# Kernel tuning notes

Hardware: AMD Instinct MI355X
Metric: run time of the kernel (lower is better)

Reference implementation:

```python
import jax, jax.numpy as jnp
import numpy as np

B, S, D, H = 2, 2048, 1024, 16
DH = D // H  # 64


def _rotate_half(t):
    x1, x2 = jnp.split(t, 2, axis=-1)
    return jnp.concatenate([-x2, x1], axis=-1)


def setup_inputs() -> dict:
    key = jax.random.key(0)
    ks = jax.random.split(key, 11)
    x = jax.random.normal(ks[0], (B, S, D), dtype=jnp.float32)
    mask = jax.random.randint(ks[1], (B, S), 0, 2, dtype=jnp.int32)
    scale = 0.02
    wq = jax.random.normal(ks[2], (D, D), dtype=jnp.float32) * scale
    bq = jnp.zeros((D,), dtype=jnp.float32)
    wk = jax.random.normal(ks[3], (D, D), dtype=jnp.float32) * scale
    bk = jnp.zeros((D,), dtype=jnp.float32)
    wv = jax.random.normal(ks[4], (D, D), dtype=jnp.float32) * scale
    bv = jnp.zeros((D,), dtype=jnp.float32)
    wo = jax.random.normal(ks[5], (D, D), dtype=jnp.float32) * scale
    bo = jnp.zeros((D,), dtype=jnp.float32)
    return {"x": x, "mask": mask, "wq": wq, "bq": bq, "wk": wk, "bk": bk,
            "wv": wv, "bv": bv, "wo": wo, "bo": bo}


def reference(x, mask, wq, bq, wk, bk, wv, bv, wo, bo):
    b, s, d = x.shape
    # QKV projections, split heads -> [B, H, S, DH]
    q = (x @ wq + bq).reshape(b, s, H, DH).transpose(0, 2, 1, 3)
    k = (x @ wk + bk).reshape(b, s, H, DH).transpose(0, 2, 1, 3)
    v = (x @ wv + bv).reshape(b, s, H, DH).transpose(0, 2, 1, 3)
    # RoPE exactly as in source: repeat(cos,2) paired with half-split rotate
    pos = jnp.arange(s, dtype=jnp.float32)
    inv_freq = 1.0 / (10000.0 ** (jnp.arange(0, DH, 2, dtype=jnp.float32) / DH))
    angle = pos[:, None] * inv_freq[None, :]            # [S, DH/2]
    cos = jnp.repeat(jnp.cos(angle), 2, axis=-1)[None, None]  # [1,1,S,DH]
    sin = jnp.repeat(jnp.sin(angle), 2, axis=-1)[None, None]
    q = q * cos + _rotate_half(q) * sin
    k = k * cos + _rotate_half(k) * sin
    # scaled dot-product attention with additive mask
    logits = jnp.einsum('bhqd,bhkd->bhqk', q, k) / jnp.sqrt(jnp.float32(DH))
    m = mask.astype(jnp.float32)[:, None, None, :]      # [B,1,1,S]
    logits = logits + m * (-1e9)
    attn = jax.nn.softmax(logits, axis=-1)
    out = jnp.einsum('bhqk,bhkd->bhqd', attn, v)
    out = out.transpose(0, 2, 1, 3).reshape(b, s, d)
    return out @ wo + bo
```

## Files before the change

### kernel.cpp

```cpp
#include <hip/hip_runtime.h>
#include <math.h>

#define BB 2
#define SS 2048
#define DD 1024
#define HH 16

typedef unsigned short u16;
using bf16x8 = __attribute__((ext_vector_type(8))) short;
using f32x4  = __attribute__((ext_vector_type(4))) float;

#define LOG2E 1.44269504f


__device__ __forceinline__ u16 f2bf(float f) {
    unsigned u = __float_as_uint(f);
    unsigned r = u + 0x7fffu + ((u >> 16) & 1u);
    return (u16)(r >> 16);
}

__device__ __forceinline__ void gload_lds16(const void* g, const void* l) {
    __builtin_amdgcn_global_load_lds(
        (const __attribute__((address_space(1))) unsigned int*)(unsigned long long)g,
        (__attribute__((address_space(3))) unsigned int*)(unsigned int)(unsigned long long)l,
        16, 0, 0);
}

__global__ void rope_table(float* __restrict__ cost, float* __restrict__ sint) {
    int idx = blockIdx.x * 256 + threadIdx.x;
    int j   = idx >> 11;
    int pos = idx & 2047;
    double inv = pow(10000.0, -(double)j / 32.0);
    double ang = (double)pos * inv;
    cost[idx] = (float)cos(ang);
    sint[idx] = (float)sin(ang);
}

__global__ void mkbias(const int* __restrict__ mask, float* __restrict__ mb) {
    int i = blockIdx.x * 256 + threadIdx.x;
    mb[i] = -1.44269504e9f * (float)mask[i];
}

__global__ void cvt_x(const float* __restrict__ x, u16* __restrict__ xb) {
    int i = (blockIdx.x * 256 + threadIdx.x) * 4;
    float4 v = *(const float4*)(x + i);
    ushort4 o;
    o.x = f2bf(v.x); o.y = f2bf(v.y); o.z = f2bf(v.z); o.w = f2bf(v.w);
    *(ushort4*)(xb + i) = o;
}

__global__ void transpose_w(const float* __restrict__ w0, const float* __restrict__ w1,
                            const float* __restrict__ w2, const float* __restrict__ w3,
                            u16* __restrict__ o0, u16* __restrict__ o1,
                            u16* __restrict__ o2, u16* __restrict__ o3) {
    const float* in = (blockIdx.z == 0) ? w0 : (blockIdx.z == 1) ? w1 : (blockIdx.z == 2) ? w2 : w3;
    u16* out        = (blockIdx.z == 0) ? o0 : (blockIdx.z == 1) ? o1 : (blockIdx.z == 2) ? o2 : o3;
    __shared__ float t[32][33];
    int n = blockIdx.x * 32 + threadIdx.x;
    for (int i = threadIdx.y; i < 32; i += 8)
        t[i][threadIdx.x] = in[(size_t)(blockIdx.y * 32 + i) * 1024 + n];
    __syncthreads();
    int k = blockIdx.y * 32 + threadIdx.x;
    for (int i = threadIdx.y; i < 32; i += 8)
        out[(size_t)(blockIdx.x * 32 + i) * 1024 + k] = f2bf(t[threadIdx.x][i]);
}

__global__ __launch_bounds__(256)
void qkv_gemm(const u16* __restrict__ xb,
              const u16* __restrict__ wtq, const u16* __restrict__ wtk, const u16* __restrict__ wtv,
              const float* __restrict__ bq, const float* __restrict__ bk, const float* __restrict__ bv,
              const float* __restrict__ cost, const float* __restrict__ sint,
              u16* __restrict__ qo, u16* __restrict__ ko, u16* __restrict__ vo)
{
    __shared__ u16 Al[128 * 32];
    __shared__ u16 Bl[128 * 32];

    int bx = blockIdx.x;
    int which = bx >> 3;
    int n0 = (bx & 7) << 7;
    int m0 = blockIdx.y << 7;
    const u16*  wt    = (which == 0) ? wtq : (which == 1) ? wtk : wtv;
    const float* bias = (which == 0) ? bq  : (which == 1) ? bk  : bv;

    int t = threadIdx.x;
    int wid = t >> 6, lane = t & 63;
    int wr = wid >> 1, wc = wid & 1;
    int fr = lane & 15, fq = lane >> 4;

    f32x4 acc[4][4];
    #pragma unroll
    for (int m = 0; m < 4; ++m)
        #pragma unroll
        for (int n = 0; n < 4; ++n)
            #pragma unroll
            for (int r = 0; r < 4; ++r) acc[m][n][r] = 0.f;

    int srow = (lane >> 2);
    int skof = (lane & 3) << 3;

    for (int k0 = 0; k0 < 1024; k0 += 32) {
        __syncthreads();
        #pragma unroll
        for (int c = 0; c < 2; ++c) {
            int chunk = wid * 2 + c;
            int row = (chunk << 4) + srow;
            gload_lds16(xb + (size_t)(m0 + row) * 1024 + k0 + skof, &Al[chunk << 9]);
            gload_lds16(wt + (size_t)(n0 + row) * 1024 + k0 + skof, &Bl[chunk << 9]);
        }
        __syncthreads();

        bf16x8 af[4], bf[4];
        #pragma unroll
        for (int m = 0; m < 4; ++m)
            af[m] = *(const bf16x8*)&Al[((wr << 6) + (m << 4) + fr) * 32 + (fq << 3)];
        #pragma unroll
        for (int n = 0; n < 4; ++n)
            bf[n] = *(const bf16x8*)&Bl[((wc << 6) + (n << 4) + fr) * 32 + (fq << 3)];
        #pragma unroll
        for (int m = 0; m < 4; ++m)
            #pragma unroll
            for (int n = 0; n < 4; ++n)
                acc[m][n] = __builtin_amdgcn_mfma_f32_16x16x32_bf16(af[m], bf[n], acc[m][n], 0, 0, 0);
    }

    if (which < 2) {
        u16* outp = (which == 0) ? qo : ko;
        const float qs = (which == 0) ? 0.125f * LOG2E : 1.0f;
        #pragma unroll
        for (int n = 0; n < 2; ++n) {
            int col = n0 + (wc << 6) + (n << 4) + fr;
            int h = col >> 6;
            int d = col & 63;
            float b1 = bias[col], b2 = bias[col + 32];
            int a1 = d >> 1;
            #pragma unroll
            for (int mm = 0; mm < 4; ++mm) {
                int mi0 = m0 + (wr << 6) + (mm << 4) + (fq << 2);
                int bi = mi0 >> 11, s0 = mi0 & 2047;
                float4 c1 = *(const float4*)(cost + (a1 << 11) + s0);
                float4 s1 = *(const float4*)(sint + (a1 << 11) + s0);
                float4 c2 = *(const float4*)(cost + ((a1 + 16) << 11) + s0);
                float4 s2 = *(const float4*)(sint + ((a1 + 16) << 11) + s0);
                const float* c1p = (const float*)&c1;
                const float* s1p = (const float*)&s1;
                const float* c2p = (const float*)&c2;
                const float* s2p = (const float*)&s2;
                #pragma unroll
                for (int j = 0; j < 4; ++j) {
                    float x1 = acc[mm][n][j]     + b1;
                    float x2 = acc[mm][n + 2][j] + b2;
                    size_t base = ((size_t)(bi * HH + h) * SS + s0 + j) << 6;
                    outp[base + d]      = f2bf((x1 * c1p[j] - x2 * s1p[j]) * qs);
                    outp[base + d + 32] = f2bf((x2 * c2p[j] + x1 * s2p[j]) * qs);
                }
            }
        }
    } else {
        #pragma unroll
        for (int n = 0; n < 4; ++n) {
            int col = n0 + (wc << 6) + (n << 4) + fr;
            int h = col >> 6, d = col & 63;
            float bb = bias[col];
            #pragma unroll
            for (int mm = 0; mm < 4; ++mm) {
                #pragma unroll
                for (int j = 0; j < 4; ++j) {
                    int mi = m0 + (wr << 6) + (mm << 4) + (fq << 2) + j;
                    int bi = mi >> 11, s = mi & 2047;
                    vo[(((size_t)(bi * HH + h) * SS + s) << 6) + d] = f2bf(acc[mm][n][j] + bb);
                }
            }
        }
    }
}

__global__ __launch_bounds__(256)
void transpose_v(const u16* __restrict__ vin, u16* __restrict__ vout) {
    __shared__ u16 Ld[64][72];
    int stile = blockIdx.x;
    int bh    = blockIdx.y;
    int t = threadIdx.x;
    int r = t >> 2, seg = (t & 3) << 4;
    const u16* src = vin + (((size_t)bh * SS + (stile << 6) + r) << 6) + seg;
    *(uint4*)&Ld[r][seg]     = *(const uint4*)src;
    *(uint4*)&Ld[r][seg + 8] = *(const uint4*)(src + 8);
    __syncthreads();
    u16 tmp[16];
    #pragma unroll
    for (int i = 0; i < 16; ++i) tmp[i] = Ld[seg + i][r];
    u16* dst = vout + ((size_t)(bh << 6) + r) * SS + (stile << 6) + seg;
    *(uint4*)dst       = *(const uint4*)&tmp[0];
    *(uint4*)(dst + 8) = *(const uint4*)&tmp[8];
}

__global__ __launch_bounds__(256, 4)
void attn(const u16* __restrict__ qb, const u16* __restrict__ kb, const u16* __restrict__ vt,
          const float* __restrict__ mbias, u16* __restrict__ preb)
{
    __shared__ u16 Kl[2][4096];
    __shared__ u16 Vl[2][4096];
    __shared__ u16 Pl[4][1024];

    const int bid = blockIdx.x;
    const int xcd = bid & 7;
    const int idx = bid >> 3;
    const int bh  = (xcd << 2) | (idx >> 5);
    const int qb0 = (idx & 31) << 6;
    const int b   = bh >> 4;
    const int t   = threadIdx.x;
    const int w   = t >> 6;
    const int lane = t & 63;
    const int fr  = lane & 15;
    const int fq  = lane >> 4;
    const int swz = (fr & 7) << 4;

    const char* kbase = (const char*)(kb + ((size_t)bh << 17));
    const char* vbase = (const char*)(vt + ((size_t)bh << 17));
    const float* mbp  = mbias + (b << 11);

    const int sbo = ((t & 7) << 4) ^ (((t >> 3) & 7) << 4);

    const int qrow = qb0 + (w << 4) + fr;
    const u16* qp = qb + (((size_t)bh << 11) + qrow) * 64 + (fq << 3);
    bf16x8 qf0 = *(const bf16x8*)qp;
    bf16x8 qf1 = *(const bf16x8*)(qp + 32);

    f32x4 o[4];
    #pragma unroll
    for (int n = 0; n < 4; ++n)
        #pragma unroll
        for (int r = 0; r < 4; ++r) o[n][r] = 0.f;
    float mrun = -INFINITY, lrun = 0.f;

    auto STAGE = [&](int buf, int kt) {
        #pragma unroll
        for (int c = 0; c < 2; ++c) {
            int row = (c << 5) + (t >> 3);
            gload_lds16(kbase + ((size_t)(kt << 6) + row) * 128 + sbo,
                        (const char*)&Kl[buf][0] + (c << 12) + t * 16);
            gload_lds16(vbase + (size_t)row * 4096 + (kt << 7) + sbo,
                        (const char*)&Vl[buf][0] + (c << 12) + t * 16);
        }
    };

    STAGE(0, 0);
    __syncthreads();

    for (int kt = 0; kt < 32; ++kt) {
        const int cur = kt & 1;

        if (kt < 31) STAGE(cur ^ 1, kt + 1);

        f32x4 sv[4];
        #pragma unroll
        for (int g = 0; g < 4; ++g)
            #pragma unroll
            for (int r = 0; r < 4; ++r) sv[g][r] = 0.f;

        const char* Kb = (const char*)&Kl[cur][0];
        __builtin_amdgcn_s_setprio(1);
        #pragma unroll
        for (int g = 0; g < 4; ++g) {
            int row = (g << 4) + fr;
            bf16x8 kf0 = *(const bf16x8*)(Kb + row * 128 + ((fq << 4) ^ swz));
            bf16x8 kf1 = *(const bf16x8*)(Kb + row * 128 + (((fq << 4) + 64) ^ swz));
            sv[g] = __builtin_amdgcn_mfma_f32_16x16x32_bf16(kf0, qf0, sv[g], 0, 0, 0);
            sv[g] = __builtin_amdgcn_mfma_f32_16x16x32_bf16(kf1, qf1, sv[g], 0, 0, 0);
        }
        __builtin_amdgcn_s_setprio(0);

        float tm = -INFINITY;
        #pragma unroll
        for (int g = 0; g < 4; ++g) {
            const float4 m4 = *(const float4*)(mbp + (kt << 6) + (g << 4) + (fq << 2));
            sv[g][0] += m4.x; sv[g][1] += m4.y; sv[g][2] += m4.z; sv[g][3] += m4.w;
            tm = fmaxf(tm, fmaxf(fmaxf(sv[g][0], sv[g][1]), fmaxf(sv[g][2], sv[g][3])));
        }
        tm = fmaxf(tm, __shfl_xor(tm, 16));
        tm = fmaxf(tm, __shfl_xor(tm, 32));

        if (!__all(tm <= mrun + 11.0f)) {
            float newm = fmaxf(mrun, tm);
            float scale = __builtin_amdgcn_exp2f(mrun - newm);
            lrun *= scale;
            #pragma unroll
            for (int j = 0; j < 4; ++j) {
                float sj = __shfl(scale, (lane & 48) + (fq << 2) + j);
                #pragma unroll
                for (int n = 0; n < 4; ++n) o[n][j] *= sj;
            }
            mrun = newm;
        }

        float ps = 0.f;
        #pragma unroll
        for (int g = 0; g < 4; ++g) {
            float p0 = __builtin_amdgcn_exp2f(sv[g][0] - mrun);
            float p1 = __builtin_amdgcn_exp2f(sv[g][1] - mrun);
            float p2 = __builtin_amdgcn_exp2f(sv[g][2] - mrun);
            float p3 = __builtin_amdgcn_exp2f(sv[g][3] - mrun);
            ps += (p0 + p1) + (p2 + p3);
            unsigned r0, r1;
            asm("v_cvt_pk_bf16_f32 %0, %1, %2" : "=v"(r0) : "v"(p0), "v"(p1));
            asm("v_cvt_pk_bf16_f32 %0, %1, %2" : "=v"(r1) : "v"(p2), "v"(p3));
            uint2 pw; pw.x = r0; pw.y = r1;
            *(uint2*)((char*)&Pl[w][0] + fr * 128 + (((g << 5) + (fq << 3)) ^ swz)) = pw;
        }
        ps += __shfl_xor(ps, 16);
        ps += __shfl_xor(ps, 32);
        lrun += ps;

        __builtin_amdgcn_s_setprio(1);
        #pragma unroll
        for (int kk = 0; kk < 2; ++kk) {
            bf16x8 pa = *(const bf16x8*)((const char*)&Pl[w][0] + fr * 128 + (((fq << 4) + (kk << 6)) ^ swz));
            #pragma unroll
            for (int n = 0; n < 4; ++n) {
                int row = (n << 4) + fr;
                bf16x8 vf = *(const bf16x8*)((const char*)&Vl[cur][0] + row * 128 + (((fq << 4) + (kk << 6)) ^ swz));
                o[n] = __builtin_amdgcn_mfma_f32_16x16x32_bf16(pa, vf, o[n], 0, 0, 0);
            }
        }
        __builtin_amdgcn_s_setprio(0);
        __syncthreads();
    }

    #pragma unroll
    for (int j = 0; j < 4; ++j) {
        float lj = __shfl(lrun, (lane & 48) + (fq << 2) + j);
        float inv = 1.0f / lj;
        int qr = qb0 + (w << 4) + (fq << 2) + j;
        u16* op = preb + ((size_t)((b << 11) + qr) << 10) + ((bh & 15) << 6) + fr;
        #pragma unroll
        for (int n = 0; n < 4; ++n)
            op[n << 4] = f2bf(o[n][j] * inv);
    }
}

__global__ __launch_bounds__(256)
void out_gemm(const u16* __restrict__ pre, const u16* __restrict__ wto,
              const float* __restrict__ bo, float* __restrict__ outp)
{
    __shared__ u16 Al[128 * 32];
    __shared__ u16 Bl[128 * 32];

    int n0 = blockIdx.x << 7;
    int m0 = blockIdx.y << 7;

    int t = threadIdx.x;
    int wid = t >> 6, lane = t & 63;
    int wr = wid >> 1, wc = wid & 1;
    int fr = lane & 15, fq = lane >> 4;

    f32x4 acc[4][4];
    #pragma unroll
    for (int m = 0; m < 4; ++m)
        #pragma unroll
        for (int n = 0; n < 4; ++n)
            #pragma unroll
            for (int r = 0; r < 4; ++r) acc[m][n][r] = 0.f;

    int srow = (lane >> 2);
    int skof = (lane & 3) << 3;

    for (int k0 = 0; k0 < 1024; k0 += 32) {
        __syncthreads();
        #pragma unroll
        for (int c = 0; c < 2; ++c) {
            int chunk = wid * 2 + c;
            int row = (chunk << 4) + srow;
            gload_lds16(pre + (size_t)(m0 + row) * 1024 + k0 + skof, &Al[chunk << 9]);
            gload_lds16(wto + (size_t)(n0 + row) * 1024 + k0 + skof, &Bl[chunk << 9]);
        }
        __syncthreads();

        bf16x8 af[4], bf[4];
        #pragma unroll
        for (int m = 0; m < 4; ++m)
            af[m] = *(const bf16x8*)&Al[((wr << 6) + (m << 4) + fr) * 32 + (fq << 3)];
        #pragma unroll
        for (int n = 0; n < 4; ++n)
            bf[n] = *(const bf16x8*)&Bl[((wc << 6) + (n << 4) + fr) * 32 + (fq << 3)];
        #pragma unroll
        for (int m = 0; m < 4; ++m)
            #pragma unroll
            for (int n = 0; n < 4; ++n)
                acc[m][n] = __builtin_amdgcn_mfma_f32_16x16x32_bf16(af[m], bf[n], acc[m][n], 0, 0, 0);
    }

    #pragma unroll
    for (int n = 0; n < 4; ++n) {
        int col = n0 + (wc << 6) + (n << 4) + fr;
        float bb = bo[col];
        #pragma unroll
        for (int m = 0; m < 4; ++m) {
            #pragma unroll
            for (int j = 0; j < 4; ++j) {
                int mi = m0 + (wr << 6) + (m << 4) + (fq << 2) + j;
                outp[(size_t)mi * 1024 + col] = acc[m][n][j] + bb;
            }
        }
    }
}

extern "C" void kernel_launch(void* const* d_in, const int* in_sizes, int n_in,
                              void* d_out, int out_size, void* d_ws, size_t ws_size,
                              hipStream_t stream) {
    const float* x    = (const float*)d_in[0];
    const int*   mask = (const int*)  d_in[1];
    const float* wq   = (const float*)d_in[2];
    const float* bq   = (const float*)d_in[3];
    const float* wk   = (const float*)d_in[4];
    const float* bk   = (const float*)d_in[5];
    const float* wv   = (const float*)d_in[6];
    const float* bv   = (const float*)d_in[7];
    const float* wo   = (const float*)d_in[8];
    const float* bo   = (const float*)d_in[9];
    float* out = (float*)d_out;
    float* ws  = (float*)d_ws;

    float* cosT  = ws;
    float* sinT  = ws + 65536;
    float* mbias = ws + 131072;
    u16* xb    = (u16*)(ws + 135168);
    u16* wtq   = xb    + 4194304;
    u16* wtk   = wtq   + 1048576;
    u16* wtv   = wtk   + 1048576;
    u16* wto   = wtv   + 1048576;
    u16* qbuf  = wto   + 1048576;
    u16* kbuf  = qbuf  + 4194304;
    u16* vbuf  = kbuf  + 4194304;
    u16* preb  = vbuf  + 4194304;
    u16* vtbuf = xb;

    hipLaunchKernelGGL(rope_table, dim3(256), dim3(256), 0, stream, cosT, sinT);
    hipLaunchKernelGGL(mkbias, dim3(16), dim3(256), 0, stream, mask, mbias);
    hipLaunchKernelGGL(cvt_x, dim3(4096), dim3(256), 0, stream, x, xb);
    hipLaunchKernelGGL(transpose_w, dim3(32, 32, 4), dim3(32, 8), 0, stream,
                       wq, wk, wv, wo, wtq, wtk, wtv, wto);
    hipLaunchKernelGGL(qkv_gemm, dim3(24, 32), dim3(256), 0, stream,
                       xb, wtq, wtk, wtv, bq, bk, bv, cosT, sinT, qbuf, kbuf, vbuf);
    hipLaunchKernelGGL(transpose_v, dim3(32, 32), dim3(256), 0, stream, vbuf, vtbuf);
    hipLaunchKernelGGL(attn, dim3(1024), dim3(256), 0, stream,
                       qbuf, kbuf, vtbuf, mbias, preb);
    hipLaunchKernelGGL(out_gemm, dim3(8, 32), dim3(256), 0, stream, preb, wto, bo, out);
}
```

Measured before the change: 241.4 us.

## Restructure attention to 32 query rows per wave with direct-to-register K/V loads

```diff
diff --git a/kernel.cpp b/kernel.cpp
--- a/kernel.cpp
+++ b/kernel.cpp
@@ -26,27 +26,29 @@
         16, 0, 0);
 }
 
-__global__ void rope_table(float* __restrict__ cost, float* __restrict__ sint) {
-    int idx = blockIdx.x * 256 + threadIdx.x;
-    int j   = idx >> 11;
-    int pos = idx & 2047;
-    double inv = pow(10000.0, -(double)j / 32.0);
-    double ang = (double)pos * inv;
-    cost[idx] = (float)cos(ang);
-    sint[idx] = (float)sin(ang);
-}
-
-__global__ void mkbias(const int* __restrict__ mask, float* __restrict__ mb) {
-    int i = blockIdx.x * 256 + threadIdx.x;
-    mb[i] = -1.44269504e9f * (float)mask[i];
-}
-
-__global__ void cvt_x(const float* __restrict__ x, u16* __restrict__ xb) {
-    int i = (blockIdx.x * 256 + threadIdx.x) * 4;
-    float4 v = *(const float4*)(x + i);
-    ushort4 o;
-    o.x = f2bf(v.x); o.y = f2bf(v.y); o.z = f2bf(v.z); o.w = f2bf(v.w);
-    *(ushort4*)(xb + i) = o;
+__global__ void prep(const float* __restrict__ x, u16* __restrict__ xb,
+                     float* __restrict__ cost, float* __restrict__ sint,
+                     const int* __restrict__ mask, float* __restrict__ mb) {
+    int gid = blockIdx.x * 256 + threadIdx.x;
+    {
+        int i = gid * 4;
+        float4 v = *(const float4*)(x + i);
+        ushort4 o;
+        o.x = f2bf(v.x); o.y = f2bf(v.y); o.z = f2bf(v.z); o.w = f2bf(v.w);
+        *(ushort4*)(xb + i) = o;
+    }
+    if (blockIdx.x < 256) {
+        int j   = gid >> 11;
+        int pos = gid & 2047;
+        double inv = pow(10000.0, -(double)j / 32.0);
+        double ang = (double)pos * inv;
+        cost[gid] = (float)cos(ang);
+        sint[gid] = (float)sin(ang);
+    }
+    if (blockIdx.x >= 256 && blockIdx.x < 272) {
+        int i = gid - 65536;
+        mb[i] = -1.44269504e9f * (float)mask[i];
+    }
 }
 
 __global__ void transpose_w(const float* __restrict__ w0, const float* __restrict__ w1,
@@ -193,19 +195,17 @@
     *(uint4*)(dst + 8) = *(const uint4*)&tmp[8];
 }
 
-__global__ __launch_bounds__(256, 4)
+__global__ __launch_bounds__(256)
 void attn(const u16* __restrict__ qb, const u16* __restrict__ kb, const u16* __restrict__ vt,
           const float* __restrict__ mbias, u16* __restrict__ preb)
 {
-    __shared__ u16 Kl[2][4096];
-    __shared__ u16 Vl[2][4096];
-    __shared__ u16 Pl[4][1024];
+    __shared__ u16 Pl[4][2048];
 
     const int bid = blockIdx.x;
     const int xcd = bid & 7;
     const int idx = bid >> 3;
-    const int bh  = (xcd << 2) | (idx >> 5);
-    const int qb0 = (idx & 31) << 6;
+    const int bh  = (xcd << 2) | (idx >> 4);
+    const int qb0 = (idx & 15) << 7;
     const int b   = bh >> 4;
     const int t   = threadIdx.x;
     const int w   = t >> 6;
@@ -214,126 +214,166 @@
     const int fq  = lane >> 4;
     const int swz = (fr & 7) << 4;
 
-    const char* kbase = (const char*)(kb + ((size_t)bh << 17));
-    const char* vbase = (const char*)(vt + ((size_t)bh << 17));
-    const float* mbp  = mbias + (b << 11);
-
-    const int sbo = ((t & 7) << 4) ^ (((t >> 3) & 7) << 4);
-
-    const int qrow = qb0 + (w << 4) + fr;
-    const u16* qp = qb + (((size_t)bh << 11) + qrow) * 64 + (fq << 3);
-    bf16x8 qf0 = *(const bf16x8*)qp;
-    bf16x8 qf1 = *(const bf16x8*)(qp + 32);
-
-    f32x4 o[4];
-    #pragma unroll
-    for (int n = 0; n < 4; ++n)
-        #pragma unroll
-        for (int r = 0; r < 4; ++r) o[n][r] = 0.f;
-    float mrun = -INFINITY, lrun = 0.f;
-
-    auto STAGE = [&](int buf, int kt) {
-        #pragma unroll
-        for (int c = 0; c < 2; ++c) {
-            int row = (c << 5) + (t >> 3);
-            gload_lds16(kbase + ((size_t)(kt << 6) + row) * 128 + sbo,
-                        (const char*)&Kl[buf][0] + (c << 12) + t * 16);
-            gload_lds16(vbase + (size_t)row * 4096 + (kt << 7) + sbo,
-                        (const char*)&Vl[buf][0] + (c << 12) + t * 16);
-        }
-    };
-
-    STAGE(0, 0);
-    __syncthreads();
+    const u16* kbase = kb + ((size_t)bh << 17);
+    const u16* vbase = vt + ((size_t)bh << 17);
+    const float* mbp = mbias + (b << 11);
+    char* Pw = (char*)&Pl[w][0];
+
+    const int qrow0 = qb0 + (w << 5);
+    bf16x8 qf[2][2];
+    #pragma unroll
+    for (int h = 0; h < 2; ++h) {
+        const u16* qp = qb + (((size_t)bh << 11) + qrow0 + (h << 4) + fr) * 64 + (fq << 3);
+        qf[h][0] = *(const bf16x8*)qp;
+        qf[h][1] = *(const bf16x8*)(qp + 32);
+    }
+
+    f32x4 o[2][4];
+    #pragma unroll
+    for (int h = 0; h < 2; ++h)
+        #pragma unroll
+        for (int n = 0; n < 4; ++n)
+            #pragma unroll
+            for (int r = 0; r < 4; ++r) o[h][n][r] = 0.f;
+    float mrun[2] = {-INFINITY, -INFINITY};
+    float lrun[2] = {0.f, 0.f};
+
+    const u16* kp = kbase + (size_t)fr * 64 + (fq << 3);
+
+    bf16x8 kc[4][2];
+    #pragma unroll
+    for (int g = 0; g < 4; ++g) {
+        const u16* p = kp + ((size_t)(g << 4) << 6);
+        kc[g][0] = *(const bf16x8*)p;
+        kc[g][1] = *(const bf16x8*)(p + 32);
+    }
 
     for (int kt = 0; kt < 32; ++kt) {
-        const int cur = kt & 1;
-
-        if (kt < 31) STAGE(cur ^ 1, kt + 1);
-
-        f32x4 sv[4];
+        f32x4 sv[4][2];
         #pragma unroll
         for (int g = 0; g < 4; ++g)
             #pragma unroll
-            for (int r = 0; r < 4; ++r) sv[g][r] = 0.f;
-
-        const char* Kb = (const char*)&Kl[cur][0];
+            for (int h = 0; h < 2; ++h)
+                #pragma unroll
+                for (int r = 0; r < 4; ++r) sv[g][h][r] = 0.f;
+
         __builtin_amdgcn_s_setprio(1);
         #pragma unroll
         for (int g = 0; g < 4; ++g) {
-            int row = (g << 4) + fr;
-            bf16x8 kf0 = *(const bf16x8*)(Kb + row * 128 + ((fq << 4) ^ swz));
-            bf16x8 kf1 = *(const bf16x8*)(Kb + row * 128 + (((fq << 4) + 64) ^ swz));
-            sv[g] = __builtin_amdgcn_mfma_f32_16x16x32_bf16(kf0, qf0, sv[g], 0, 0, 0);
-            sv[g] = __builtin_amdgcn_mfma_f32_16x16x32_bf16(kf1, qf1, sv[g], 0, 0, 0);
+            #pragma unroll
+            for (int h = 0; h < 2; ++h) {
+                sv[g][h] = __builtin_amdgcn_mfma_f32_16x16x32_bf16(kc[g][0], qf[h][0], sv[g][h], 0, 0, 0);
+                sv[g][h] = __builtin_amdgcn_mfma_f32_16x16x32_bf16(kc[g][1], qf[h][1], sv[g][h], 0, 0, 0);
+            }
         }
         __builtin_amdgcn_s_setprio(0);
 
-        float tm = -INFINITY;
+        const int ktn = (kt + 1) & 31;
+        bf16x8 kn[4][2];
+        #pragma unroll
+        for (int g = 0; g < 4; ++g) {
+            const u16* p = kp + ((size_t)((ktn << 6) + (g << 4)) << 6);
+            kn[g][0] = *(const bf16x8*)p;
+            kn[g][1] = *(const bf16x8*)(p + 32);
+        }
+        bf16x8 vfr[2][4];
+        #pragma unroll
+        for (int kk = 0; kk < 2; ++kk)
+            #pragma unroll
+            for (int n = 0; n < 4; ++n)
+                vfr[kk][n] = *(const bf16x8*)(vbase + (((size_t)(n << 4) + fr) << 11)
+                                              + (kt << 6) + (kk << 5) + (fq << 3));
+
+        float tm[2] = {-INFINITY, -INFINITY};
         #pragma unroll
         for (int g = 0; g < 4; ++g) {
             const float4 m4 = *(const float4*)(mbp + (kt << 6) + (g << 4) + (fq << 2));
-            sv[g][0] += m4.x; sv[g][1] += m4.y; sv[g][2] += m4.z; sv[g][3] += m4.w;
-            tm = fmaxf(tm, fmaxf(fmaxf(sv[g][0], sv[g][1]), fmaxf(sv[g][2], sv[g][3])));
-        }
-        tm = fmaxf(tm, __shfl_xor(tm, 16));
-        tm = fmaxf(tm, __shfl_xor(tm, 32));
-
-        if (!__all(tm <= mrun + 11.0f)) {
-            float newm = fmaxf(mrun, tm);
-            float scale = __builtin_amdgcn_exp2f(mrun - newm);
-            lrun *= scale;
-            #pragma unroll
-            for (int j = 0; j < 4; ++j) {
-                float sj = __shfl(scale, (lane & 48) + (fq << 2) + j);
+            #pragma unroll
+            for (int h = 0; h < 2; ++h) {
+                sv[g][h][0] += m4.x; sv[g][h][1] += m4.y;
+                sv[g][h][2] += m4.z; sv[g][h][3] += m4.w;
+                tm[h] = fmaxf(tm[h], fmaxf(fmaxf(sv[g][h][0], sv[g][h][1]),
+                                           fmaxf(sv[g][h][2], sv[g][h][3])));
+            }
+        }
+        #pragma unroll
+        for (int h = 0; h < 2; ++h) {
+            tm[h] = fmaxf(tm[h], __shfl_xor(tm[h], 16));
+            tm[h] = fmaxf(tm[h], __shfl_xor(tm[h], 32));
+        }
+
+        if (!__all(tm[0] <= mrun[0] + 11.0f && tm[1] <= mrun[1] + 11.0f)) {
+            #pragma unroll
+            for (int h = 0; h < 2; ++h) {
+                float newm = fmaxf(mrun[h], tm[h]);
+                float scale = __builtin_amdgcn_exp2f(mrun[h] - newm);
+                lrun[h] *= scale;
                 #pragma unroll
-                for (int n = 0; n < 4; ++n) o[n][j] *= sj;
-            }
-            mrun = newm;
-        }
-
-        float ps = 0.f;
+                for (int j = 0; j < 4; ++j) {
+                    float sj = __shfl(scale, (lane & 48) + (fq << 2) + j);
+                    #pragma unroll
+                    for (int n = 0; n < 4; ++n) o[h][n][j] *= sj;
+                }
+                mrun[h] = newm;
+            }
+        }
+
+        #pragma unroll
+        for (int h = 0; h < 2; ++h) {
+            float ps = 0.f;
+            #pragma unroll
+            for (int g = 0; g < 4; ++g) {
+                float p0 = __builtin_amdgcn_exp2f(sv[g][h][0] - mrun[h]);
+                float p1 = __builtin_amdgcn_exp2f(sv[g][h][1] - mrun[h]);
+                float p2 = __builtin_amdgcn_exp2f(sv[g][h][2] - mrun[h]);
+                float p3 = __builtin_amdgcn_exp2f(sv[g][h][3] - mrun[h]);
+                ps += (p0 + p1) + (p2 + p3);
+                unsigned r0, r1;
+                asm("v_cvt_pk_bf16_f32 %0, %1, %2" : "=v"(r0) : "v"(p0), "v"(p1));
+                asm("v_cvt_pk_bf16_f32 %0, %1, %2" : "=v"(r1) : "v"(p2), "v"(p3));
+                uint2 pw; pw.x = r0; pw.y = r1;
+                *(uint2*)(Pw + (fr + (h << 4)) * 128 + (((g << 5) + (fq << 3)) ^ swz)) = pw;
+            }
+            ps += __shfl_xor(ps, 16);
+            ps += __shfl_xor(ps, 32);
+            lrun[h] += ps;
+        }
+
+        __builtin_amdgcn_s_setprio(1);
+        #pragma unroll
+        for (int kk = 0; kk < 2; ++kk) {
+            bf16x8 pa[2];
+            #pragma unroll
+            for (int h = 0; h < 2; ++h)
+                pa[h] = *(const bf16x8*)(Pw + (fr + (h << 4)) * 128 + (((kk << 6) + (fq << 4)) ^ swz));
+            #pragma unroll
+            for (int n = 0; n < 4; ++n) {
+                #pragma unroll
+                for (int h = 0; h < 2; ++h)
+                    o[h][n] = __builtin_amdgcn_mfma_f32_16x16x32_bf16(pa[h], vfr[kk][n], o[h][n], 0, 0, 0);
+            }
+        }
+        __builtin_amdgcn_s_setprio(0);
+
         #pragma unroll
         for (int g = 0; g < 4; ++g) {
-            float p0 = __builtin_amdgcn_exp2f(sv[g][0] - mrun);
-            float p1 = __builtin_amdgcn_exp2f(sv[g][1] - mrun);
-            float p2 = __builtin_amdgcn_exp2f(sv[g][2] - mrun);
-            float p3 = __builtin_amdgcn_exp2f(sv[g][3] - mrun);
-            ps += (p0 + p1) + (p2 + p3);
-            unsigned r0, r1;
-            asm("v_cvt_pk_bf16_f32 %0, %1, %2" : "=v"(r0) : "v"(p0), "v"(p1));
-            asm("v_cvt_pk_bf16_f32 %0, %1, %2" : "=v"(r1) : "v"(p2), "v"(p3));
-            uint2 pw; pw.x = r0; pw.y = r1;
-            *(uint2*)((char*)&Pl[w][0] + fr * 128 + (((g << 5) + (fq << 3)) ^ swz)) = pw;
-        }
-        ps += __shfl_xor(ps, 16);
-        ps += __shfl_xor(ps, 32);
-        lrun += ps;
-
-        __builtin_amdgcn_s_setprio(1);
-        #pragma unroll
-        for (int kk = 0; kk < 2; ++kk) {
-            bf16x8 pa = *(const bf16x8*)((const char*)&Pl[w][0] + fr * 128 + (((fq << 4) + (kk << 6)) ^ swz));
-            #pragma unroll
-            for (int n = 0; n < 4; ++n) {
-                int row = (n << 4) + fr;
-                bf16x8 vf = *(const bf16x8*)((const char*)&Vl[cur][0] + row * 128 + (((fq << 4) + (kk << 6)) ^ swz));
-                o[n] = __builtin_amdgcn_mfma_f32_16x16x32_bf16(pa, vf, o[n], 0, 0, 0);
-            }
-        }
-        __builtin_amdgcn_s_setprio(0);
-        __syncthreads();
-    }
-
-    #pragma unroll
-    for (int j = 0; j < 4; ++j) {
-        float lj = __shfl(lrun, (lane & 48) + (fq << 2) + j);
-        float inv = 1.0f / lj;
-        int qr = qb0 + (w << 4) + (fq << 2) + j;
-        u16* op = preb + ((size_t)((b << 11) + qr) << 10) + ((bh & 15) << 6) + fr;
-        #pragma unroll
-        for (int n = 0; n < 4; ++n)
-            op[n << 4] = f2bf(o[n][j] * inv);
+            kc[g][0] = kn[g][0];
+            kc[g][1] = kn[g][1];
+        }
+    }
+
+    #pragma unroll
+    for (int h = 0; h < 2; ++h) {
+        #pragma unroll
+        for (int j = 0; j < 4; ++j) {
+            float lj = __shfl(lrun[h], (lane & 48) + (fq << 2) + j);
+            float inv = 1.0f / lj;
+            int qr = qrow0 + (h << 4) + (fq << 2) + j;
+            u16* op = preb + ((size_t)((b << 11) + qr) << 10) + ((bh & 15) << 6) + fr;
+            #pragma unroll
+            for (int n = 0; n < 4; ++n)
+                op[n << 4] = f2bf(o[h][n][j] * inv);
+        }
     }
 }
 
@@ -433,15 +473,13 @@
     u16* preb  = vbuf  + 4194304;
     u16* vtbuf = xb;
 
-    hipLaunchKernelGGL(rope_table, dim3(256), dim3(256), 0, stream, cosT, sinT);
-    hipLaunchKernelGGL(mkbias, dim3(16), dim3(256), 0, stream, mask, mbias);
-    hipLaunchKernelGGL(cvt_x, dim3(4096), dim3(256), 0, stream, x, xb);
+    hipLaunchKernelGGL(prep, dim3(4096), dim3(256), 0, stream, x, xb, cosT, sinT, mask, mbias);
     hipLaunchKernelGGL(transpose_w, dim3(32, 32, 4), dim3(32, 8), 0, stream,
                        wq, wk, wv, wo, wtq, wtk, wtv, wto);
     hipLaunchKernelGGL(qkv_gemm, dim3(24, 32), dim3(256), 0, stream,
                        xb, wtq, wtk, wtv, bq, bk, bv, cosT, sinT, qbuf, kbuf, vbuf);
     hipLaunchKernelGGL(transpose_v, dim3(32, 32), dim3(256), 0, stream, vbuf, vtbuf);
-    hipLaunchKernelGGL(attn, dim3(1024), dim3(256), 0, stream,
+    hipLaunchKernelGGL(attn, dim3(512), dim3(256), 0, stream,
                        qbuf, kbuf, vtbuf, mbias, preb);
     hipLaunchKernelGGL(out_gemm, dim3(8, 32), dim3(256), 0, stream, preb, wto, bo, out);
 }
```

Result: slower. 303.5 us (+25.7%).
